# Optimization experiments

Hardware: AMD Instinct MI355X
Metric: run time of the kernel (lower is better)

## Reference

```python
import jax, jax.numpy as jnp
import numpy as np

RANK = 3
NUM_STEPS = 3
NUM_ENT = 40000
NUM_EMB = 24
NUM_OPS = 12
DIM = 128
HID = 128
BATCH = 128
NNZ = 300000


def _lstm_dir(x, Wih, Whh, bih, bhh, reverse=False):
    # x: (S, B, D); PyTorch gate order i, f, g, o
    B = x.shape[1]
    H = Whh.shape[1]
    def step(carry, xt):
        h, c = carry
        z = xt @ Wih.T + h @ Whh.T + bih + bhh  # (B, 4H)
        i, f, g, o = jnp.split(z, 4, axis=-1)
        c = jax.nn.sigmoid(f) * c + jax.nn.sigmoid(i) * jnp.tanh(g)
        h = jax.nn.sigmoid(o) * jnp.tanh(c)
        return (h, c), h
    init = (jnp.zeros((B, H), x.dtype), jnp.zeros((B, H), x.dtype))
    _, hs = jax.lax.scan(step, init, x, reverse=reverse)
    return hs  # (S, B, H)


def _spmm(memory, src, dst, val, num_ent):
    # memory: (B, E); edges (src -> dst): out[b, j] = sum_{e: dst[e]=j} memory[b, src[e]] * val[e]
    g = memory[:, src] * val[None, :]              # (B, nnz)
    out = jax.ops.segment_sum(g.T, dst, num_segments=num_ent)  # (E, B)
    return out.T


def setup_inputs() -> dict:
    key = jax.random.key(0)
    ks = jax.random.split(key, 16)
    inp = {
        'queries': jax.random.randint(ks[0], (BATCH,), 0, NUM_EMB),
        'heads': jax.random.randint(ks[1], (BATCH,), 0, NUM_ENT),
        'edge_src': jax.random.randint(ks[2], (NUM_OPS, NNZ), 0, NUM_ENT, dtype=jnp.int32),
        'edge_dst': jax.random.randint(ks[3], (NUM_OPS, NNZ), 0, NUM_ENT, dtype=jnp.int32),
        'edge_val': jax.random.uniform(ks[4], (NUM_OPS, NNZ), jnp.float32),
        'emb': jax.random.normal(ks[5], (NUM_EMB, DIM), jnp.float32) * 0.1,
        'Wih_f': jax.random.normal(ks[6], (RANK, 4 * HID, DIM), jnp.float32) * 0.1,
        'Whh_f': jax.random.normal(ks[7], (RANK, 4 * HID, HID), jnp.float32) * 0.1,
        'bih_f': jnp.zeros((RANK, 4 * HID), jnp.float32),
        'bhh_f': jnp.zeros((RANK, 4 * HID), jnp.float32),
        'Wih_b': jax.random.normal(ks[8], (RANK, 4 * HID, DIM), jnp.float32) * 0.1,
        'Whh_b': jax.random.normal(ks[9], (RANK, 4 * HID, HID), jnp.float32) * 0.1,
        'bih_b': jnp.zeros((RANK, 4 * HID), jnp.float32),
        'bhh_b': jnp.zeros((RANK, 4 * HID), jnp.float32),
        'W0': jax.random.normal(ks[10], (2 * HID, NUM_OPS + 1), jnp.float32) * 0.1,
        'b0': jnp.zeros((1, NUM_OPS + 1), jnp.float32),
    }
    return inp


def reference(queries, heads, edge_src, edge_dst, edge_val, emb,
              Wih_f, Whh_f, bih_f, bhh_f, Wih_b, Whh_b, bih_b, bhh_b, W0, b0):
    # query embedding replicated over time: (S, B, D)
    q = emb[queries]
    x = jnp.broadcast_to(q[None], (NUM_STEPS, q.shape[0], q.shape[1]))
    head_onehot = jax.nn.one_hot(heads, NUM_ENT, dtype=jnp.float32)  # (B, E)

    logits = jnp.zeros((q.shape[0], NUM_ENT), jnp.float32)
    for r in range(RANK):
        hf = _lstm_dir(x, Wih_f[r], Whh_f[r], bih_f[r], bhh_f[r], reverse=False)
        hb = _lstm_dir(x, Wih_b[r], Whh_b[r], bih_b[r], bhh_b[r], reverse=True)
        rnn_out = jnp.concatenate([hf, hb], axis=-1)          # (S, B, 2H)
        trans = rnn_out @ W0 + b0                             # (S, B, ops+1)
        attn = jax.nn.softmax(trans, axis=-1)
        attn = jnp.transpose(attn, (0, 2, 1))                 # (S, ops+1, B)

        memory = head_onehot                                  # (B, E)
        for t in range(NUM_STEPS):
            attn_t = attn[t]                                  # (ops+1, B)
            acc = memory * attn_t[-1][:, None]                # identity operator
            for op in range(NUM_OPS):
                prod = _spmm(memory, edge_src[op], edge_dst[op], edge_val[op], NUM_ENT)
                acc = acc + prod * attn_t[op][:, None]
            memory = acc
        norm = jnp.maximum(jnp.float32(1e-20), jnp.sum(memory, axis=1, keepdims=True))
        logits = logits + memory / norm
    return logits
```

## Files before the change

kernel.cpp:

```cpp
#include <hip/hip_runtime.h>

#define NENT 40000
#define NB 128
#define NQ 24
#define NOPS 12
#define EPO 300000
#define NTOT (NOPS * EPO)
#define NRANK 3
#define NPASS 8
#define CP 16
#define ECAP 160

typedef float v4f __attribute__((ext_vector_type(4)));

__device__ __forceinline__ v4f shfl_xor4(v4f x, int m) {
    v4f r;
    r.x = __shfl_xor(x.x, m);
    r.y = __shfl_xor(x.y, m);
    r.z = __shfl_xor(x.z, m);
    r.w = __shfl_xor(x.w, m);
    return r;
}

__device__ __forceinline__ bool bittest(const unsigned* bm, int i) {
    return (bm[i >> 5] >> (i & 31)) & 1u;
}

__global__ void headmark_kernel(const int* __restrict__ heads, unsigned* __restrict__ bmH,
                                unsigned* __restrict__ bm2) {
    int h = heads[threadIdx.x];
    atomicOr(&bmH[h >> 5], 1u << (h & 31));
    atomicOr(&bm2[h >> 5], 1u << (h & 31));
}

__global__ void mark2_kernel(const int* __restrict__ src, const int* __restrict__ dst,
                             const unsigned* __restrict__ bmH, unsigned* __restrict__ bm2) {
    int i = blockIdx.x * 256 + threadIdx.x;
    if (i < NTOT) {
        int s = src[i];
        if (bittest(bmH, s)) {
            int d = dst[i];
            atomicOr(&bm2[d >> 5], 1u << (d & 31));
        }
    }
}

__global__ void build_ell_kernel(const int* __restrict__ src, const int* __restrict__ dst,
                                 const float* __restrict__ val, const unsigned* __restrict__ bm2,
                                 int* __restrict__ fillD, int* __restrict__ fillS,
                                 int2* __restrict__ eD, int2* __restrict__ eS) {
    int i = blockIdx.x * 256 + threadIdx.x;
    if (i >= NTOT) return;
    int s = src[i], d = dst[i];
    int op = i / EPO;
    int v = __float_as_int(val[i]);
    int pd = atomicAdd(&fillD[d], 1);
    eD[(size_t)d * ECAP + pd] = make_int2(s | (op << 16), v);
    if (bittest(bm2, s)) {
        int ps = atomicAdd(&fillS[s], 1);
        eS[(size_t)s * ECAP + ps] = make_int2(d | (op << 16), v);
    }
}

__global__ void lstm_all_kernel(const float* __restrict__ emb,
                                const float* __restrict__ Wih_f, const float* __restrict__ bih_f,
                                const float* __restrict__ bhh_f,
                                const float* __restrict__ Wih_b, const float* __restrict__ bih_b,
                                const float* __restrict__ bhh_b,
                                const float* __restrict__ Whh_f, const float* __restrict__ Whh_b,
                                float* __restrict__ hq) {
    int combo = blockIdx.x / NQ;
    int q = blockIdx.x % NQ;
    int dir = combo / 3, r = combo % 3;
    const float* Wih = (dir ? Wih_b : Wih_f) + r * 512 * 128;
    const float* bih = (dir ? bih_b : bih_f) + r * 512;
    const float* bhh = (dir ? bhh_b : bhh_f) + r * 512;
    const float* Whh = (dir ? Whh_b : Whh_f) + r * 512 * 128;
    __shared__ float x[128];
    __shared__ float h[128];
    int u = threadIdx.x;
    x[u] = emb[q * 128 + u];
    __syncthreads();
    const float* W0p = Wih + u * 128;
    const float* W1p = Wih + (128 + u) * 128;
    const float* W2p = Wih + (256 + u) * 128;
    const float* W3p = Wih + (384 + u) * 128;
    float a0 = 0.f, a1 = 0.f, a2 = 0.f, a3 = 0.f;
    for (int d = 0; d < 128; ++d) {
        float xv = x[d];
        a0 = fmaf(xv, W0p[d], a0);
        a1 = fmaf(xv, W1p[d], a1);
        a2 = fmaf(xv, W2p[d], a2);
        a3 = fmaf(xv, W3p[d], a3);
    }
    float zi0 = a0 + bih[u]       + bhh[u];
    float zf0 = a1 + bih[128 + u] + bhh[128 + u];
    float zg0 = a2 + bih[256 + u] + bhh[256 + u];
    float zo0 = a3 + bih[384 + u] + bhh[384 + u];
    const float* Wi = Whh + u * 128;
    const float* Wf = Whh + (128 + u) * 128;
    const float* Wg = Whh + (256 + u) * 128;
    const float* Wo = Whh + (384 + u) * 128;
    float c = 0.f;
    h[u] = 0.f;
    for (int s = 0; s < 3; ++s) {
        __syncthreads();
        float b0 = 0.f, b1 = 0.f, b2 = 0.f, b3 = 0.f;
        for (int d = 0; d < 128; ++d) {
            float hv = h[d];
            b0 = fmaf(hv, Wi[d], b0);
            b1 = fmaf(hv, Wf[d], b1);
            b2 = fmaf(hv, Wg[d], b2);
            b3 = fmaf(hv, Wo[d], b3);
        }
        float ig = 1.f / (1.f + expf(-(zi0 + b0)));
        float fg = 1.f / (1.f + expf(-(zf0 + b1)));
        float gg = tanhf(zg0 + b2);
        float og = 1.f / (1.f + expf(-(zo0 + b3)));
        c = fg * c + ig * gg;
        float hn = og * tanhf(c);
        __syncthreads();
        h[u] = hn;
        hq[(size_t)((combo * 3 + s) * NQ + q) * 128 + u] = hn;
    }
}

__global__ void attnq_kernel(const float* __restrict__ hq, const float* __restrict__ W0,
                             const float* __restrict__ b0, float* __restrict__ attnq) {
    int r = blockIdx.x / 3, t = blockIdx.x % 3;
    __shared__ float W0s[256 * 13];
    for (int idx = threadIdx.x; idx < 256 * 13; idx += 128) W0s[idx] = W0[idx];
    __syncthreads();
    int q = threadIdx.x;
    if (q >= NQ) return;
    float acc[13];
    for (int k = 0; k < 13; ++k) acc[k] = b0[k];
    const float* hf = hq + (size_t)(((0 * 3 + r) * 3 + t) * NQ + q) * 128;
    const float* hb = hq + (size_t)(((1 * 3 + r) * 3 + (2 - t)) * NQ + q) * 128;
    for (int u = 0; u < 128; ++u) {
        float v = hf[u];
        for (int k = 0; k < 13; ++k) acc[k] = fmaf(v, W0s[u * 13 + k], acc[k]);
    }
    for (int u = 0; u < 128; ++u) {
        float v = hb[u];
        for (int k = 0; k < 13; ++k) acc[k] = fmaf(v, W0s[(128 + u) * 13 + k], acc[k]);
    }
    float m = acc[0];
    for (int k = 1; k < 13; ++k) m = fmaxf(m, acc[k]);
    float e[13];
    float sum = 0.f;
    for (int k = 0; k < 13; ++k) { e[k] = expf(acc[k] - m); sum += e[k]; }
    float inv = 1.f / sum;
    float* ao = attnq + (size_t)(r * 3 + t) * 13 * NQ;
    for (int k = 0; k < 13; ++k) ao[k * NQ + q] = e[k] * inv;
}

__global__ void fused01_kernel(const int* __restrict__ heads, const int* __restrict__ queries,
                               const float* __restrict__ attnq,
                               const int* __restrict__ fillS, const int2* __restrict__ eS,
                               float* __restrict__ mem2) {
    int r = blockIdx.y;
    int b = blockIdx.x;
    int chunk = blockIdx.z;
    __shared__ float c0s[13], c1s[13];
    if (threadIdx.x < 13) {
        int qb = queries[b];
        c0s[threadIdx.x] = attnq[(size_t)((r * 3 + 0) * 13 + threadIdx.x) * NQ + qb];
        c1s[threadIdx.x] = attnq[(size_t)((r * 3 + 1) * 13 + threadIdx.x) * NQ + qb];
    }
    __syncthreads();
    int h = heads[b];
    int lenH = fillS[h];
    float* mem = mem2 + ((size_t)(r * NPASS + (b >> 4)) * NENT) * CP + (b & 15);
    int g = threadIdx.x >> 3, lane8 = threadIdx.x & 7;
    for (int ent = g + chunk * 32; ent < lenH + 1; ent += 64) {
        int i; float wv;
        if (ent == 0) { i = h; wv = c0s[12]; }
        else {
            int2 e = eS[(size_t)h * ECAP + ent - 1];
            i = e.x & 0xFFFF;
            wv = __int_as_float(e.y) * c0s[e.x >> 16];
        }
        if (lane8 == 0) atomicAdd(&mem[(size_t)i * CP], c1s[12] * wv);
        int lenI = fillS[i];
        const int2* ei = eS + (size_t)i * ECAP;
        for (int f = lane8; f < lenI; f += 8) {
            int2 e2 = ei[f];
            atomicAdd(&mem[(size_t)(e2.x & 0xFFFF) * CP],
                      __int_as_float(e2.y) * c1s[e2.x >> 16] * wv);
        }
    }
}

__global__ __launch_bounds__(256) void dense_kernel(const int* __restrict__ queries,
                                                    const float* __restrict__ attnq,
                                                    const int* __restrict__ fillD,
                                                    const int2* __restrict__ edgesD,
                                                    const float* __restrict__ in,
                                                    float* __restrict__ out,
                                                    float* __restrict__ normv) {
    int p = blockIdx.x;
    int r = blockIdx.z;
    __shared__ __align__(16) float cs[13 * 20];
    __shared__ float npart[4][16];
    int tid = threadIdx.x;
    if (tid < 13 * 16) {
        int op = tid >> 4, c0 = tid & 15;
        cs[op * 20 + c0] = attnq[(size_t)((r * 3 + 2) * 13 + op) * NQ + queries[p * CP + c0]];
    }
    __syncthreads();
    int wave = tid >> 6, lane = tid & 63;
    int slot = lane >> 2;
    int cq4 = (lane & 3) * 4;
    int jw = blockIdx.y * 16 + wave * 4;
    const float* inr = in + (size_t)(r * NPASS + p) * NENT * CP;
    float* outr = out + (size_t)(r * NPASS + p) * NENT * CP;
    int lens[4];
    const int2* edp[4];
#pragma unroll
    for (int t = 0; t < 4; ++t) {
        lens[t] = fillD[jw + t];
        edp[t] = edgesD + (size_t)(jw + t) * ECAP;
    }
    int maxlen = max(max(lens[0], lens[1]), max(lens[2], lens[3]));
    v4f acc[4];
#pragma unroll
    for (int t = 0; t < 4; ++t) acc[t] = (v4f)0.f;

    for (int base = 0; base < maxlen; base += 32) {
        int2 e[8];
        bool m[8];
#pragma unroll
        for (int t = 0; t < 4; ++t) {
            int ia = base + slot;
            int ib = base + 16 + slot;
            m[t]     = ia < lens[t];
            m[4 + t] = ib < lens[t];
            e[t]     = edp[t][m[t] ? ia : 0];
            e[4 + t] = edp[t][m[4 + t] ? ib : 0];
        }
        v4f g[8];
#pragma unroll
        for (int u = 0; u < 8; ++u)
            g[u] = *(const v4f*)(inr + (size_t)(e[u].x & 0xFFFF) * CP + cq4);
#pragma unroll
        for (int u = 0; u < 8; ++u) {
            v4f cc = *(const v4f*)&cs[(e[u].x >> 16) * 20 + cq4];
            float v = m[u] ? __int_as_float(e[u].y) : 0.f;
            acc[u & 3] += (v * cc) * g[u];
        }
    }

    v4f cid = *(const v4f*)&cs[12 * 20 + cq4];
    v4f rsum = (v4f)0.f;
#pragma unroll
    for (int t = 0; t < 4; ++t) {
        v4f red = acc[t];
        red += shfl_xor4(red, 4);
        red += shfl_xor4(red, 8);
        red += shfl_xor4(red, 16);
        red += shfl_xor4(red, 32);
        if (slot == 0) {
            int j = jw + t;
            v4f mi = *(const v4f*)(inr + (size_t)j * CP + cq4);
            v4f res = cid * mi + red;
            *(v4f*)(outr + (size_t)j * CP + cq4) = res;
            rsum += res;
        }
    }
    if (slot == 0) *(v4f*)&npart[wave][cq4] = rsum;
    __syncthreads();
    if (tid < 16) {
        float s = npart[0][tid] + npart[1][tid] + npart[2][tid] + npart[3][tid];
        atomicAdd(&normv[r * 128 + p * CP + tid], s);
    }
}

__global__ void final_kernel(const float* __restrict__ mem3, const float* __restrict__ normv,
                             float* __restrict__ out) {
    __shared__ float tile[32 * 129];
    __shared__ float rn[384];
    for (int idx = threadIdx.x; idx < 384; idx += 256)
        rn[idx] = 1.f / fmaxf(normv[idx], 1e-20f);
    __syncthreads();
    int j0 = blockIdx.x * 32;
    for (int p = 0; p < NPASS; ++p) {
        for (int it = 0; it < 2; ++it) {
            int lin = it * 256 + threadIdx.x;
            int jj = lin >> 4, c = lin & 15;
            int b = p * CP + c;
            float s = 0.f;
            for (int r = 0; r < 3; ++r)
                s += mem3[((size_t)(r * NPASS + p) * NENT + j0 + jj) * CP + c] * rn[r * 128 + b];
            tile[jj * 129 + b] = s;
        }
    }
    __syncthreads();
    for (int it = 0; it < 16; ++it) {
        int lin = it * 256 + threadIdx.x;
        int b = lin >> 5, jj = lin & 31;
        out[(size_t)b * NENT + j0 + jj] = tile[jj * 129 + b];
    }
}

extern "C" void kernel_launch(void* const* d_in, const int* in_sizes, int n_in,
                              void* d_out, int out_size, void* d_ws, size_t ws_size,
                              hipStream_t stream) {
    const int*   queries  = (const int*)d_in[0];
    const int*   heads    = (const int*)d_in[1];
    const int*   edge_src = (const int*)d_in[2];
    const int*   edge_dst = (const int*)d_in[3];
    const float* edge_val = (const float*)d_in[4];
    const float* emb      = (const float*)d_in[5];
    const float* Wih_f    = (const float*)d_in[6];
    const float* Whh_f    = (const float*)d_in[7];
    const float* bih_f    = (const float*)d_in[8];
    const float* bhh_f    = (const float*)d_in[9];
    const float* Wih_b    = (const float*)d_in[10];
    const float* Whh_b    = (const float*)d_in[11];
    const float* bih_b    = (const float*)d_in[12];
    const float* bhh_b    = (const float*)d_in[13];
    const float* W0       = (const float*)d_in[14];
    const float* b0       = (const float*)d_in[15];
    float* out = (float*)d_out;

    char* w = (char*)d_ws;
    size_t off = 0;
    auto alloc = [&](size_t bytes) -> void* {
        off = (off + 255) & ~(size_t)255;
        void* p = w + off;
        off += bytes;
        return p;
    };
    float* attnq  = (float*)alloc((size_t)9 * 13 * NQ * sizeof(float));
    float* hq     = (float*)alloc((size_t)6 * 3 * NQ * 128 * sizeof(float));
    unsigned* bmH = (unsigned*)alloc((2 * 1250 + 2 * NENT) * sizeof(int));
    unsigned* bm2 = bmH + 1250;
    int* fillD    = (int*)(bm2 + 1250);
    int* fillS    = fillD + NENT;
    int2*  eD     = (int2*)alloc((size_t)NENT * ECAP * sizeof(int2));
    float* mem2   = (float*)alloc((size_t)NRANK * NENT * NB * sizeof(float));
    float* mem3   = (float*)alloc((size_t)NRANK * NENT * NB * sizeof(float));
    int2*  eS     = (int2*)mem3;
    float* normv  = (float*)alloc((size_t)NRANK * NB * sizeof(float));

    int cooGrid = (NTOT + 255) / 256;

    hipMemsetAsync(bmH, 0, (2 * 1250 + 2 * NENT) * sizeof(int), stream);
    headmark_kernel<<<1, 128, 0, stream>>>(heads, bmH, bm2);
    mark2_kernel<<<cooGrid, 256, 0, stream>>>(edge_src, edge_dst, bmH, bm2);
    build_ell_kernel<<<cooGrid, 256, 0, stream>>>(edge_src, edge_dst, edge_val, bm2,
                                                  fillD, fillS, eD, eS);

    lstm_all_kernel<<<6 * NQ, 128, 0, stream>>>(emb, Wih_f, bih_f, bhh_f,
                                                Wih_b, bih_b, bhh_b, Whh_f, Whh_b, hq);
    attnq_kernel<<<9, 128, 0, stream>>>(hq, W0, b0, attnq);

    hipMemsetAsync(mem2, 0, (size_t)NRANK * NENT * NB * sizeof(float), stream);
    hipMemsetAsync(normv, 0, NRANK * NB * sizeof(float), stream);
    {
        dim3 g(NB, NRANK, 2);
        fused01_kernel<<<g, 256, 0, stream>>>(heads, queries, attnq, fillS, eS, mem2);
    }
    {
        dim3 g(NPASS, NENT / 16, NRANK);
        dense_kernel<<<g, 256, 0, stream>>>(queries, attnq, fillD, eD, mem2, mem3, normv);
    }

    final_kernel<<<NENT / 32, 256, 0, stream>>>(mem3, normv, out);
}
```

Measured before the change: 1.294 ms.

## Sort destination rows by in-degree to balance dense SpMM wave work

Adds a counting sort of destination entities by in-degree (histogram, serial prefix, scatter) and has the dense kernel process rows in that order. Each wave then handles four rows of similar length, so the loop bound set by the longest row wastes fewer iterations. It also clamps masked edge gathers to row 0. The cost is three extra small launches, a single-threaded prefix, and scattered row writes and identity reads in the dense kernel.

```diff
diff --git a/kernel.cpp b/kernel.cpp
--- a/kernel.cpp
+++ b/kernel.cpp
@@ -59,6 +59,28 @@
     if (bittest(bm2, s)) {
         int ps = atomicAdd(&fillS[s], 1);
         eS[(size_t)s * ECAP + ps] = make_int2(d | (op << 16), v);
+    }
+}
+
+__global__ void hist_kernel(const int* __restrict__ fillD, int* __restrict__ hist) {
+    int j = blockIdx.x * 256 + threadIdx.x;
+    if (j < NENT) atomicAdd(&hist[min(fillD[j], 160)], 1);
+}
+
+__global__ void prefix_kernel(const int* __restrict__ hist, int* __restrict__ offs) {
+    if (threadIdx.x == 0) {
+        int s = 0;
+        for (int l = 0; l <= 160; ++l) { offs[l] = s; s += hist[l]; }
+    }
+}
+
+__global__ void scatter_kernel(const int* __restrict__ fillD, int* __restrict__ offs,
+                               int* __restrict__ perm) {
+    int j = blockIdx.x * 256 + threadIdx.x;
+    if (j < NENT) {
+        int l = min(fillD[j], 160);
+        int p = atomicAdd(&offs[l], 1);
+        perm[p] = j;
     }
 }
 
@@ -195,6 +217,7 @@
 __global__ __launch_bounds__(256) void dense_kernel(const int* __restrict__ queries,
                                                     const float* __restrict__ attnq,
                                                     const int* __restrict__ fillD,
+                                                    const int* __restrict__ perm,
                                                     const int2* __restrict__ edgesD,
                                                     const float* __restrict__ in,
                                                     float* __restrict__ out,
@@ -212,15 +235,16 @@
     int wave = tid >> 6, lane = tid & 63;
     int slot = lane >> 2;
     int cq4 = (lane & 3) * 4;
-    int jw = blockIdx.y * 16 + wave * 4;
+    int jb = blockIdx.y * 16 + wave * 4;
     const float* inr = in + (size_t)(r * NPASS + p) * NENT * CP;
     float* outr = out + (size_t)(r * NPASS + p) * NENT * CP;
-    int lens[4];
+    int jr[4], lens[4];
     const int2* edp[4];
 #pragma unroll
     for (int t = 0; t < 4; ++t) {
-        lens[t] = fillD[jw + t];
-        edp[t] = edgesD + (size_t)(jw + t) * ECAP;
+        jr[t] = perm[jb + t];
+        lens[t] = fillD[jr[t]];
+        edp[t] = edgesD + (size_t)jr[t] * ECAP;
     }
     int maxlen = max(max(lens[0], lens[1]), max(lens[2], lens[3]));
     v4f acc[4];
@@ -241,8 +265,10 @@
         }
         v4f g[8];
 #pragma unroll
-        for (int u = 0; u < 8; ++u)
-            g[u] = *(const v4f*)(inr + (size_t)(e[u].x & 0xFFFF) * CP + cq4);
+        for (int u = 0; u < 8; ++u) {
+            int row = m[u] ? (e[u].x & 0xFFFF) : 0;
+            g[u] = *(const v4f*)(inr + (size_t)row * CP + cq4);
+        }
 #pragma unroll
         for (int u = 0; u < 8; ++u) {
             v4f cc = *(const v4f*)&cs[(e[u].x >> 16) * 20 + cq4];
@@ -261,7 +287,7 @@
         red += shfl_xor4(red, 16);
         red += shfl_xor4(red, 32);
         if (slot == 0) {
-            int j = jw + t;
+            int j = jr[t];
             v4f mi = *(const v4f*)(inr + (size_t)j * CP + cq4);
             v4f res = cid * mi + red;
             *(v4f*)(outr + (size_t)j * CP + cq4) = res;
@@ -334,10 +360,13 @@
     };
     float* attnq  = (float*)alloc((size_t)9 * 13 * NQ * sizeof(float));
     float* hq     = (float*)alloc((size_t)6 * 3 * NQ * 128 * sizeof(float));
-    unsigned* bmH = (unsigned*)alloc((2 * 1250 + 2 * NENT) * sizeof(int));
+    unsigned* bmH = (unsigned*)alloc((2 * 1250 + 2 * NENT + 161) * sizeof(int));
     unsigned* bm2 = bmH + 1250;
     int* fillD    = (int*)(bm2 + 1250);
     int* fillS    = fillD + NENT;
+    int* hist     = fillS + NENT;
+    int* offs     = (int*)alloc(161 * sizeof(int));
+    int* perm     = (int*)alloc((size_t)NENT * sizeof(int));
     int2*  eD     = (int2*)alloc((size_t)NENT * ECAP * sizeof(int2));
     float* mem2   = (float*)alloc((size_t)NRANK * NENT * NB * sizeof(float));
     float* mem3   = (float*)alloc((size_t)NRANK * NENT * NB * sizeof(float));
@@ -345,12 +374,17 @@
     float* normv  = (float*)alloc((size_t)NRANK * NB * sizeof(float));
 
     int cooGrid = (NTOT + 255) / 256;
-
-    hipMemsetAsync(bmH, 0, (2 * 1250 + 2 * NENT) * sizeof(int), stream);
+    int entGrid = (NENT + 255) / 256;
+
+    hipMemsetAsync(bmH, 0, (2 * 1250 + 2 * NENT + 161) * sizeof(int), stream);
     headmark_kernel<<<1, 128, 0, stream>>>(heads, bmH, bm2);
     mark2_kernel<<<cooGrid, 256, 0, stream>>>(edge_src, edge_dst, bmH, bm2);
     build_ell_kernel<<<cooGrid, 256, 0, stream>>>(edge_src, edge_dst, edge_val, bm2,
                                                   fillD, fillS, eD, eS);
+
+    hist_kernel<<<entGrid, 256, 0, stream>>>(fillD, hist);
+    prefix_kernel<<<1, 64, 0, stream>>>(hist, offs);
+    scatter_kernel<<<entGrid, 256, 0, stream>>>(fillD, offs, perm);
 
     lstm_all_kernel<<<6 * NQ, 128, 0, stream>>>(emb, Wih_f, bih_f, bhh_f,
                                                 Wih_b, bih_b, bhh_b, Whh_f, Whh_b, hq);
@@ -364,7 +398,7 @@
     }
     {
         dim3 g(NPASS, NENT / 16, NRANK);
-        dense_kernel<<<g, 256, 0, stream>>>(queries, attnq, fillD, eD, mem2, mem3, normv);
+        dense_kernel<<<g, 256, 0, stream>>>(queries, attnq, fillD, perm, eD, mem2, mem3, normv);
     }
 
     final_kernel<<<NENT / 32, 256, 0, stream>>>(mem3, normv, out);
```

Result: slower. 1.335 ms (+3.2%).
